# Kernel tuning notes

Hardware: AMD Instinct MI355X
Metric: run time of the kernel (lower is better)

## Reference

```python
import jax, jax.numpy as jnp
import numpy as np

N = 100000      # n_nodes
D = 64          # in_features (= out_features)
H = 4           # attention heads
DK = D // H     # per-head dim
E = 1600000     # num edges (avg degree 16)
STEP = 0.25     # ODE euler step size
NSTEPS = 4      # integrate t in [0, 1]
ALPHA = 0.2     # LeakyReLU negative slope


def setup_inputs() -> dict:
    key = jax.random.key(0)
    k1, k2, k3, k4 = jax.random.split(key, 4)
    x = jax.random.normal(k1, (N, D), dtype=jnp.float32)
    edge_index = jax.random.randint(k2, (2, E), 0, N, dtype=jnp.int32)
    edge_weight = jax.random.uniform(k3, (E,), dtype=jnp.float32)
    # HamAgg.weight: init.eye_ -> identity [D, D]
    W = jnp.eye(D, dtype=jnp.float32)
    # HAM_GATConv.a: xavier_normal_ on shape (2*d_k, 1, 1), gain=1.414
    a = jax.random.normal(k4, (2 * DK,), dtype=jnp.float32) * (1.414 * np.sqrt(2.0 / (2 * DK + 1)))
    return {"x": x, "edge_index": edge_index, "edge_weight": edge_weight, "W": W, "a": a}


def reference(x, edge_index, edge_weight, W, a):
    # ---- Hamiltonian ODE block (args.vt == 'fc', odemap 'h1extend') ----
    # xt = hstack([x, x @ W.T]); euler-integrate canonical Hamiltonian flow
    # dq/dt = p, dp/dt = -q over t in [0,1] with step 0.25; keep first D dims.
    q = x
    p = x @ W.T
    for _ in range(NSTEPS):
        q, p = q + STEP * p, p - STEP * q
    xt = q  # out_x = out[..., :D]

    row, col = edge_index[0], edge_index[1]

    # ---- HAM_GATConv attention (W_x = x @ I = x) ----
    # h[n, head, k] = xt[n, head*DK + k]
    h = xt.reshape(N, H, DK)
    a_src, a_dst = a[:DK], a[DK:]
    s_src = h @ a_src   # [N, H] per-node source contribution
    s_dst = h @ a_dst   # [N, H] per-node dest contribution
    score = jax.nn.leaky_relu(s_src[row] + s_dst[col], ALPHA)  # [E, H]

    # segment softmax grouped by destination (edge[1])
    seg_max = jax.ops.segment_max(score, col, num_segments=N)  # [N, H]
    seg_max = jnp.where(jnp.isfinite(seg_max), seg_max, 0.0)
    e = jnp.exp(score - seg_max[col])
    denom = jax.ops.segment_sum(e, col, num_segments=N)
    att = e / (denom[col] + 1e-16)  # [E, H]

    # ---- mean over heads of per-head spmm == single spmm with mean attention ----
    # spmm: out[row[e]] += att[e] * xt[col[e]]
    w = att.mean(axis=1)  # [E]
    out = jax.ops.segment_sum(w[:, None] * xt[col], row, num_segments=N)  # [N, D]
    return out
```

## Files before the change

### kernel.cpp

```cpp
#include <hip/hip_runtime.h>
#include <hip/hip_bf16.h>


#define LRELU(v) ((v) > 0.0f ? (v) : 0.2f * (v))

#define EC 4096
#define BSC 256
#define BSR 128
#define DS 4
#define SLOTS 4

typedef __attribute__((ext_vector_type(8))) short bf16x8;
typedef __attribute__((ext_vector_type(4))) float f32x4;

__device__ __forceinline__ float bf16_to_f32(unsigned short u) {
    return __uint_as_float((unsigned int)u << 16);
}
__device__ __forceinline__ float bflo(unsigned int u) {
    return __uint_as_float(u << 16);
}
__device__ __forceinline__ float bfhi(unsigned int u) {
    return __uint_as_float(u & 0xFFFF0000u);
}
__device__ __forceinline__ unsigned short f32_to_bf16(float f) {
    __hip_bfloat16 h = __float2bfloat16(f);
    return *reinterpret_cast<unsigned short*>(&h);
}

__global__ __launch_bounds__(256) void k_front(const float* __restrict__ x,
                                               const float* __restrict__ W,
                                               const float* __restrict__ a,
                                               const int* __restrict__ row,
                                               const int* __restrict__ col,
                                               unsigned short* __restrict__ xt16,
                                               float* __restrict__ s_src,
                                               float* __restrict__ s_dst,
                                               int* __restrict__ Hr,
                                               int* __restrict__ Hc,
                                               int n, int e, int nbn, int nblk,
                                               int nbr, int nbc,
                                               float c1, float c2) {
    __shared__ unsigned short geffL[16 * 64];
    __shared__ int hr[1024];
    __shared__ int hc[512];
    int t = threadIdx.x;
    if (blockIdx.x < nbn) {
        {
            int k = t & 63, h = t >> 6;
            float ssrc = 0.0f, sdst = 0.0f;
#pragma unroll
            for (int d = 0; d < 16; ++d) {
                float w = W[(h * 16 + d) * 64 + k];
                ssrc += w * a[d];
                sdst += w * a[16 + d];
            }
            float gsrc = c2 * ssrc, gdst = c2 * sdst;
            if ((k >> 4) == h) {
                gsrc += c1 * a[k & 15];
                gdst += c1 * a[16 + (k & 15)];
            }
            unsigned short sh = f32_to_bf16(gsrc);
            unsigned short sl = f32_to_bf16(gsrc - bf16_to_f32(sh));
            unsigned short dh = f32_to_bf16(gdst);
            unsigned short dl = f32_to_bf16(gdst - bf16_to_f32(dh));
            geffL[h * 64 + k] = sh;
            geffL[(4 + h) * 64 + k] = dh;
            geffL[(8 + h) * 64 + k] = sl;
            geffL[(12 + h) * 64 + k] = dl;
        }
        __syncthreads();

        int wave = t >> 6;
        int lane = t & 63;
        int nb = blockIdx.x * 64 + wave * 16;
        if (nb >= n) return;
        int colg = lane & 15;
        int grp = lane >> 4;
        int k0 = grp << 3;

        bf16x8 wf[4][2];
#pragma unroll
        for (int ct = 0; ct < 4; ++ct) {
#pragma unroll
            for (int ks = 0; ks < 2; ++ks) {
                const float* wr = W + (size_t)(ct * 16 + colg) * 64 + k0 + ks * 32;
                float4 w0 = *(const float4*)(wr);
                float4 w1 = *(const float4*)(wr + 4);
                bf16x8 f;
                f[0] = (short)f32_to_bf16(w0.x); f[1] = (short)f32_to_bf16(w0.y);
                f[2] = (short)f32_to_bf16(w0.z); f[3] = (short)f32_to_bf16(w0.w);
                f[4] = (short)f32_to_bf16(w1.x); f[5] = (short)f32_to_bf16(w1.y);
                f[6] = (short)f32_to_bf16(w1.z); f[7] = (short)f32_to_bf16(w1.w);
                wf[ct][ks] = f;
            }
        }
        bf16x8 gf[2];
#pragma unroll
        for (int ks = 0; ks < 2; ++ks)
            gf[ks] = *(const bf16x8*)(geffL + colg * 64 + k0 + ks * 32);

        int arow = nb + colg;
        if (arow >= n) arow = n - 1;
        const float* xr = x + (size_t)arow * 64 + k0;
        bf16x8 af[2];
#pragma unroll
        for (int ks = 0; ks < 2; ++ks) {
            float4 x0 = *(const float4*)(xr + ks * 32);
            float4 x1 = *(const float4*)(xr + ks * 32 + 4);
            bf16x8 f;
            f[0] = (short)f32_to_bf16(x0.x); f[1] = (short)f32_to_bf16(x0.y);
            f[2] = (short)f32_to_bf16(x0.z); f[3] = (short)f32_to_bf16(x0.w);
            f[4] = (short)f32_to_bf16(x1.x); f[5] = (short)f32_to_bf16(x1.y);
            f[6] = (short)f32_to_bf16(x1.z); f[7] = (short)f32_to_bf16(x1.w);
            af[ks] = f;
        }

        f32x4 acc[5];
#pragma unroll
        for (int i = 0; i < 5; ++i) acc[i] = (f32x4){0.f, 0.f, 0.f, 0.f};
#pragma unroll
        for (int ct = 0; ct < 4; ++ct) {
            acc[ct] = __builtin_amdgcn_mfma_f32_16x16x32_bf16(af[0], wf[ct][0], acc[ct], 0, 0, 0);
            acc[ct] = __builtin_amdgcn_mfma_f32_16x16x32_bf16(af[1], wf[ct][1], acc[ct], 0, 0, 0);
        }
        acc[4] = __builtin_amdgcn_mfma_f32_16x16x32_bf16(af[0], gf[0], acc[4], 0, 0, 0);
        acc[4] = __builtin_amdgcn_mfma_f32_16x16x32_bf16(af[1], gf[1], acc[4], 0, 0, 0);

#pragma unroll
        for (int ct = 0; ct < 4; ++ct) {
            int c = ct * 16 + colg;
#pragma unroll
            for (int rr = 0; rr < 4; ++rr) {
                int node = nb + grp * 4 + rr;
                if (node < n) {
                    float xv = x[(size_t)node * 64 + c];
                    float xtv = c1 * xv + c2 * acc[ct][rr];
                    xt16[(size_t)node * 64 + c] = f32_to_bf16(xtv);
                }
            }
        }
#pragma unroll
        for (int rr = 0; rr < 4; ++rr) {
            float v = acc[4][rr];
            float tot = v + __shfl_xor(v, 8, 64);
            int node = nb + grp * 4 + rr;
            if (node < n) {
                if (colg < 4) s_src[node * 4 + colg] = tot;
                else if (colg < 8) s_dst[node * 4 + (colg - 4)] = tot;
            }
        }
    } else {
        int blk = blockIdx.x - nbn;
        for (int i = t; i < 1024; i += 256) hr[i] = 0;
        for (int i = t; i < 512; i += 256) hc[i] = 0;
        __syncthreads();
        int base = blk * EC;
#pragma unroll
        for (int j = 0; j < EC / 256; ++j) {
            int i = base + t + j * 256;
            if (i < e) {
                atomicAdd(&hr[row[i] >> 7], 1);
                atomicAdd(&hc[col[i] >> 8], 1);
            }
        }
        __syncthreads();
        for (int b = t; b < nbr; b += 256) Hr[(size_t)b * nblk + blk] = hr[b];
        for (int b = t; b < nbc; b += 256) Hc[(size_t)b * nblk + blk] = hc[b];
    }
}

__global__ __launch_bounds__(256) void k_scanH2(int* __restrict__ Hr,
                                                int* __restrict__ Hc,
                                                int* __restrict__ BtotR,
                                                int* __restrict__ BtotC,
                                                int nblk, int nbr) {
    __shared__ int vals[512];
    __shared__ int part[256];
    int t = threadIdx.x;
    int bb = blockIdx.x;
    int* Hb;
    int* Btot;
    if (bb < nbr) {
        Hb = Hr + (size_t)bb * nblk;
        Btot = BtotR + bb;
    } else {
        Hb = Hc + (size_t)(bb - nbr) * nblk;
        Btot = BtotC + (bb - nbr);
    }
    for (int i = t; i < nblk; i += 256) vals[i] = Hb[i];
    __syncthreads();
    int c0 = t * 2;
    int s = 0;
#pragma unroll
    for (int j = 0; j < 2; ++j)
        if (c0 + j < nblk) s += vals[c0 + j];
    part[t] = s;
    __syncthreads();
    for (int d = 1; d < 256; d <<= 1) {
        int add = (t >= d) ? part[t - d] : 0;
        __syncthreads();
        part[t] += add;
        __syncthreads();
    }
    int run = part[t] - s;
#pragma unroll
    for (int j = 0; j < 2; ++j) {
        int i = c0 + j;
        if (i < nblk) {
            int v = vals[i];
            Hb[i] = run;
            run += v;
        }
    }
    if (t == 255) *Btot = part[255];
}

__global__ __launch_bounds__(256) void k_scatter_dual(
    const int* __restrict__ row, const int* __restrict__ col,
    const int* __restrict__ Hr, const int* __restrict__ Hc,
    const int* __restrict__ BtotR, const int* __restrict__ BtotC,
    int* __restrict__ BbR, int* __restrict__ BbC,
    int* __restrict__ ebr, int* __restrict__ ebc,
    int e, int nblk, int nbr, int nbc) {
    __shared__ int vals[1024];
    __shared__ int part[256];
    __shared__ int curr[1024];
    __shared__ int curc[512];
    int t = threadIdx.x;
    int blk = blockIdx.x;
    for (int i = t; i < nbr; i += 256) vals[i] = BtotR[i];
    __syncthreads();
    {
        int c0 = t * 4, s = 0;
#pragma unroll
        for (int j = 0; j < 4; ++j)
            if (c0 + j < nbr) s += vals[c0 + j];
        part[t] = s;
        __syncthreads();
        for (int d = 1; d < 256; d <<= 1) {
            int add = (t >= d) ? part[t - d] : 0;
            __syncthreads();
            part[t] += add;
            __syncthreads();
        }
        int run = part[t] - s;
#pragma unroll
        for (int j = 0; j < 4; ++j) {
            int i = c0 + j;
            if (i < nbr) {
                int v = vals[i];
                curr[i] = run + Hr[(size_t)i * nblk + blk];
                if (blk == 0) BbR[i] = run;
                run += v;
            }
        }
        if (blk == 0 && t == 255) BbR[nbr] = part[255];
    }
    __syncthreads();
    for (int i = t; i < nbc; i += 256) vals[i] = BtotC[i];
    __syncthreads();
    {
        int c0 = t * 4, s = 0;
#pragma unroll
        for (int j = 0; j < 4; ++j)
            if (c0 + j < nbc) s += vals[c0 + j];
        part[t] = s;
        __syncthreads();
        for (int d = 1; d < 256; d <<= 1) {
            int add = (t >= d) ? part[t - d] : 0;
            __syncthreads();
            part[t] += add;
            __syncthreads();
        }
        int run = part[t] - s;
#pragma unroll
        for (int j = 0; j < 4; ++j) {
            int i = c0 + j;
            if (i < nbc) {
                int v = vals[i];
                curc[i] = run + Hc[(size_t)i * nblk + blk];
                if (blk == 0) BbC[i] = run;
                run += v;
            }
        }
        if (blk == 0 && t == 255) BbC[nbc] = part[255];
    }
    __syncthreads();
    int base = blk * EC;
#pragma unroll
    for (int j = 0; j < EC / 256; ++j) {
        int i = base + t + j * 256;
        if (i < e) {
            int r = row[i], c = col[i];
            int pr = atomicAdd(&curr[r >> 7], 1);
            ebr[pr] = (c << 7) | (r & 127);
            int pc = atomicAdd(&curc[c >> 8], 1);
            ebc[pc] = (r << 8) | (c & 255);
        }
    }
}

__global__ __launch_bounds__(256) void k_denom_p(const int* __restrict__ ebc,
                                                 const int* __restrict__ BbC,
                                                 const float* __restrict__ s_src,
                                                 const float* __restrict__ s_dst,
                                                 float* __restrict__ part,
                                                 int n, int n4) {
    __shared__ float acc[BSC * 4];
    __shared__ float sd[BSC * 4];
    int t = threadIdx.x;
    int bucket = blockIdx.x >> 2;
    int slice = blockIdx.x & 3;
    int cbase = bucket << 8;
    for (int i = t; i < BSC * 4; i += 256) {
        acc[i] = 0.0f;
        int c4 = cbase * 4 + i;
        sd[i] = (c4 < n4) ? s_dst[c4] : 0.0f;
    }
    __syncthreads();
    int start = BbC[bucket], end = BbC[bucket + 1];
    int len = end - start;
    int i0 = start + (int)(((long long)len * slice) >> 2);
    int i1 = start + (int)(((long long)len * (slice + 1)) >> 2);
    for (int i = i0 + t; i < i1; i += 256) {
        int p = ebc[i];
        int r = p >> 8, cl = p & 255;
        float4 ss = *(const float4*)(s_src + (size_t)r * 4);
        atomicAdd(&acc[cl * 4 + 0], __expf(LRELU(ss.x + sd[cl * 4 + 0])));
        atomicAdd(&acc[cl * 4 + 1], __expf(LRELU(ss.y + sd[cl * 4 + 1])));
        atomicAdd(&acc[cl * 4 + 2], __expf(LRELU(ss.z + sd[cl * 4 + 2])));
        atomicAdd(&acc[cl * 4 + 3], __expf(LRELU(ss.w + sd[cl * 4 + 3])));
    }
    __syncthreads();
    float* ps = part + (size_t)slice * n4;
    for (int i = t; i < BSC * 4; i += 256) {
        int c4 = cbase * 4 + i;
        if (c4 < n4) ps[c4] = acc[i];
    }
}

__global__ __launch_bounds__(256) void k_comb(const float* __restrict__ part,
                                              const float* __restrict__ s_dst,
                                              float* __restrict__ sdr, int n4) {
    int idx = blockIdx.x * 256 + threadIdx.x;
    if (idx >= n4) return;
    float s = part[idx] + part[(size_t)n4 + idx] + part[(size_t)2 * n4 + idx] +
              part[(size_t)3 * n4 + idx];
    int c = idx >> 2, h = idx & 3;
    sdr[(size_t)c * 8 + h] = s_dst[idx];
    sdr[(size_t)c * 8 + 4 + h] = 1.0f / (s + 1e-16f);
}

__global__ __launch_bounds__(256) void k_sort2(const int* __restrict__ ebr,
                                               const int* __restrict__ BbR,
                                               const float* __restrict__ s_src,
                                               const float* __restrict__ sdr,
                                               int* __restrict__ rowptr,
                                               int2* __restrict__ cwp,
                                               int n, int e) {
    __shared__ int cnt[BSR];
    __shared__ int pfx[BSR];
    __shared__ int cur[BSR];
    __shared__ float ssh[BSR * 4];
    int t = threadIdx.x;
    int b = blockIdx.x;
    int rbase = b << 7;
    if (t < BSR) cnt[t] = 0;
    for (int i = t; i < BSR * 4; i += 256) {
        int g = rbase * 4 + i;
        ssh[i] = (g < n * 4) ? s_src[g] : 0.0f;
    }
    __syncthreads();
    int start = BbR[b], end = BbR[b + 1];
    for (int i = start + t; i < end; i += 256)
        atomicAdd(&cnt[ebr[i] & 127], 1);
    __syncthreads();
    if (t < BSR) pfx[t] = cnt[t];
    __syncthreads();
    for (int d = 1; d < BSR; d <<= 1) {
        int v = (t < BSR && t >= d) ? pfx[t - d] : 0;
        __syncthreads();
        if (t < BSR) pfx[t] += v;
        __syncthreads();
    }
    if (t < BSR) {
        int excl = start + pfx[t] - cnt[t];
        cur[t] = excl;
        int r = rbase + t;
        if (r < n) rowptr[r] = excl;
    }
    if (b == 0 && t == 0) rowptr[n] = e;
    __syncthreads();
    for (int i = start + t; i < end; i += 256) {
        int p = ebr[i];
        int rl = p & 127, c = p >> 7;
        float4 sd = *(const float4*)(sdr + (size_t)c * 8);
        float4 rd = *(const float4*)(sdr + (size_t)c * 8 + 4);
        float wv = __expf(LRELU(ssh[rl * 4 + 0] + sd.x)) * rd.x +
                   __expf(LRELU(ssh[rl * 4 + 1] + sd.y)) * rd.y +
                   __expf(LRELU(ssh[rl * 4 + 2] + sd.z)) * rd.z +
                   __expf(LRELU(ssh[rl * 4 + 3] + sd.w)) * rd.w;
        int pos = atomicAdd(&cur[rl], 1);
        cwp[pos] = make_int2(c << 6, __float_as_int(0.25f * wv));
    }
}

__global__ __launch_bounds__(256) void k_aggr(const int* __restrict__ rowptr,
                                              const int2* __restrict__ cwp,
                                              const unsigned short* __restrict__ xt16,
                                              float* __restrict__ out, int n, int e) {
    int r = blockIdx.x * 4 + (threadIdx.x >> 6);
    if (r >= n) return;
    int lane = threadIdx.x & 63;
    int g = lane >> 3;
    unsigned le = (lane & 7) << 3;
    int start = rowptr[r], end = rowptr[r + 1];
    float acc[8];
#pragma unroll
    for (int j = 0; j < 8; ++j) acc[j] = 0.0f;
    for (int base = start; base < end; base += SLOTS * 8) {
        int m = end - base;
        if (m > SLOTS * 8) m = SLOTS * 8;
        int nk = (m + 7) >> 3;
        uint4 u[SLOTS];
        float wv[SLOTS];
#pragma unroll
        for (int k = 0; k < SLOTS; ++k) {
            if (k < nk) {
                int idx = base + k * 8 + g;
                int idc = idx < e ? idx : e - 1;
                int2 cw = cwp[idc];
                wv[k] = (idx < end) ? __int_as_float(cw.y) : 0.0f;
                u[k] = *(const uint4*)(xt16 + ((unsigned)cw.x + le));
            }
        }
#pragma unroll
        for (int k = 0; k < SLOTS; ++k) {
            if (k < nk) {
                acc[0] = fmaf(wv[k], bflo(u[k].x), acc[0]);
                acc[1] = fmaf(wv[k], bfhi(u[k].x), acc[1]);
                acc[2] = fmaf(wv[k], bflo(u[k].y), acc[2]);
                acc[3] = fmaf(wv[k], bfhi(u[k].y), acc[3]);
                acc[4] = fmaf(wv[k], bflo(u[k].z), acc[4]);
                acc[5] = fmaf(wv[k], bfhi(u[k].z), acc[5]);
                acc[6] = fmaf(wv[k], bflo(u[k].w), acc[6]);
                acc[7] = fmaf(wv[k], bfhi(u[k].w), acc[7]);
            }
        }
    }
#pragma unroll
    for (int off = 8; off <= 32; off <<= 1) {
#pragma unroll
        for (int j = 0; j < 8; ++j) acc[j] += __shfl_xor(acc[j], off, 64);
    }
    if (lane < 8) {
        float4 a0 = {acc[0], acc[1], acc[2], acc[3]};
        float4 a1 = {acc[4], acc[5], acc[6], acc[7]};
        *(float4*)(out + (size_t)r * 64 + le) = a0;
        *(float4*)(out + (size_t)r * 64 + le + 4) = a1;
    }
}

extern "C" void kernel_launch(void* const* d_in, const int* in_sizes, int n_in,
                              void* d_out, int out_size, void* d_ws, size_t ws_size,
                              hipStream_t stream) {
    const float* x = (const float*)d_in[0];
    const int* ei = (const int*)d_in[1];
    const float* W = (const float*)d_in[3];
    const float* a = (const float*)d_in[4];
    int n = in_sizes[0] / 64;
    int e = in_sizes[1] / 2;
    const int* row = ei;
    const int* col = ei + e;
    float* out = (float*)d_out;

    int nblk = (e + EC - 1) / EC;
    int nbr = (n + BSR - 1) / BSR;
    int nbc = (n + BSC - 1) / BSC;
    int nbn = (n + 63) / 64;
    int n4 = n * 4;

    size_t o = 0;
    auto take = [&](size_t cnt) {
        size_t p = o;
        o += (cnt + 3) & ~(size_t)3;
        return p;
    };
    int* wsi = (int*)d_ws;
    unsigned short* xt16 = (unsigned short*)(wsi + take((size_t)n * 32));
    float* s_src = (float*)(wsi + take((size_t)n * 4));
    float* s_dst = (float*)(wsi + take((size_t)n * 4));
    float* sdr = (float*)(wsi + take((size_t)n * 8));
    float* part = (float*)(wsi + take((size_t)n * 4 * DS));
    int* Hr = wsi + take((size_t)nbr * nblk);
    int* Hc = wsi + take((size_t)nbc * nblk);
    int* BtotR = wsi + take(nbr);
    int* BbR = wsi + take(nbr + 1);
    int* BtotC = wsi + take(nbc);
    int* BbC = wsi + take(nbc + 1);
    int* ebr = wsi + take(e);
    int* cwbuf = wsi + take((size_t)2 * e);
    int* ebc = cwbuf;
    int2* cwp = (int2*)cwbuf;
    int* rowptr = wsi + take(n + 1);

    float aq = 1.f, bq = 0.f, ap = 0.f, bp = 1.f;
    for (int i = 0; i < 4; ++i) {
        float naq = aq + 0.25f * ap, nbq = bq + 0.25f * bp;
        float nap = ap - 0.25f * aq, nbp = bp - 0.25f * bq;
        aq = naq; bq = nbq; ap = nap; bp = nbp;
    }

    k_front<<<nbn + nblk, 256, 0, stream>>>(x, W, a, row, col, xt16, s_src,
                                            s_dst, Hr, Hc, n, e, nbn, nblk,
                                            nbr, nbc, aq, bq);
    k_scanH2<<<nbr + nbc, 256, 0, stream>>>(Hr, Hc, BtotR, BtotC, nblk, nbr);
    k_scatter_dual<<<nblk, 256, 0, stream>>>(row, col, Hr, Hc, BtotR, BtotC,
                                             BbR, BbC, ebr, ebc, e, nblk,
                                             nbr, nbc);
    k_denom_p<<<nbc * DS, 256, 0, stream>>>(ebc, BbC, s_src, s_dst, part, n, n4);
    k_comb<<<(n4 + 255) / 256, 256, 0, stream>>>(part, s_dst, sdr, n4);
    k_sort2<<<nbr, 256, 0, stream>>>(ebr, BbR, s_src, sdr, rowptr, cwp, n, e);
    k_aggr<<<(n + 3) / 4, 256, 0, stream>>>(rowptr, cwp, xt16, out, n, e);
}
```

Baseline: 281.3 us.

## Halve histogram chunk size and move row counting into the denominator kernel

The edge histogram in the front kernel now uses 2048-edge chunks, giving twice as many histogram blocks for more parallelism. The scatter kernel still works on 4096-edge chunks and reads every other histogram column, and the scan kernel handles up to 1024 entries per bucket. The per-row counting and prefix-sum that used to open the sort kernel now runs as extra blocks inside the denominator kernel, so it executes concurrently with the softmax denominator work. The placement kernel then only reads the precomputed rowptr. The cost is more histogram writes, plus a second pass over ebr in a separate kernel.

```diff
diff --git a/kernel.cpp b/kernel.cpp
--- a/kernel.cpp
+++ b/kernel.cpp
@@ -5,6 +5,7 @@
 #define LRELU(v) ((v) > 0.0f ? (v) : 0.2f * (v))
 
 #define EC 4096
+#define ECH 2048
 #define BSC 256
 #define BSR 128
 #define DS 4
@@ -37,7 +38,7 @@
                                                float* __restrict__ s_dst,
                                                int* __restrict__ Hr,
                                                int* __restrict__ Hc,
-                                               int n, int e, int nbn, int nblk,
+                                               int n, int e, int nbn, int nblkH,
                                                int nbr, int nbc,
                                                float c1, float c2) {
     __shared__ unsigned short geffL[16 * 64];
@@ -154,9 +155,9 @@
         for (int i = t; i < 1024; i += 256) hr[i] = 0;
         for (int i = t; i < 512; i += 256) hc[i] = 0;
         __syncthreads();
-        int base = blk * EC;
-#pragma unroll
-        for (int j = 0; j < EC / 256; ++j) {
+        int base = blk * ECH;
+#pragma unroll
+        for (int j = 0; j < ECH / 256; ++j) {
             int i = base + t + j * 256;
             if (i < e) {
                 atomicAdd(&hr[row[i] >> 7], 1);
@@ -164,8 +165,8 @@
             }
         }
         __syncthreads();
-        for (int b = t; b < nbr; b += 256) Hr[(size_t)b * nblk + blk] = hr[b];
-        for (int b = t; b < nbc; b += 256) Hc[(size_t)b * nblk + blk] = hc[b];
+        for (int b = t; b < nbr; b += 256) Hr[(size_t)b * nblkH + blk] = hr[b];
+        for (int b = t; b < nbc; b += 256) Hc[(size_t)b * nblkH + blk] = hc[b];
     }
 }
 
@@ -173,27 +174,27 @@
                                                 int* __restrict__ Hc,
                                                 int* __restrict__ BtotR,
                                                 int* __restrict__ BtotC,
-                                                int nblk, int nbr) {
-    __shared__ int vals[512];
+                                                int nblkH, int nbr) {
+    __shared__ int vals[1024];
     __shared__ int part[256];
     int t = threadIdx.x;
     int bb = blockIdx.x;
     int* Hb;
     int* Btot;
     if (bb < nbr) {
-        Hb = Hr + (size_t)bb * nblk;
+        Hb = Hr + (size_t)bb * nblkH;
         Btot = BtotR + bb;
     } else {
-        Hb = Hc + (size_t)(bb - nbr) * nblk;
+        Hb = Hc + (size_t)(bb - nbr) * nblkH;
         Btot = BtotC + (bb - nbr);
     }
-    for (int i = t; i < nblk; i += 256) vals[i] = Hb[i];
-    __syncthreads();
-    int c0 = t * 2;
+    for (int i = t; i < nblkH; i += 256) vals[i] = Hb[i];
+    __syncthreads();
+    int c0 = t * 4;
     int s = 0;
 #pragma unroll
-    for (int j = 0; j < 2; ++j)
-        if (c0 + j < nblk) s += vals[c0 + j];
+    for (int j = 0; j < 4; ++j)
+        if (c0 + j < nblkH) s += vals[c0 + j];
     part[t] = s;
     __syncthreads();
     for (int d = 1; d < 256; d <<= 1) {
@@ -204,9 +205,9 @@
     }
     int run = part[t] - s;
 #pragma unroll
-    for (int j = 0; j < 2; ++j) {
+    for (int j = 0; j < 4; ++j) {
         int i = c0 + j;
-        if (i < nblk) {
+        if (i < nblkH) {
             int v = vals[i];
             Hb[i] = run;
             run += v;
@@ -221,13 +222,14 @@
     const int* __restrict__ BtotR, const int* __restrict__ BtotC,
     int* __restrict__ BbR, int* __restrict__ BbC,
     int* __restrict__ ebr, int* __restrict__ ebc,
-    int e, int nblk, int nbr, int nbc) {
+    int e, int nblkH, int nbr, int nbc) {
     __shared__ int vals[1024];
     __shared__ int part[256];
     __shared__ int curr[1024];
     __shared__ int curc[512];
     int t = threadIdx.x;
     int blk = blockIdx.x;
+    int hcol = blk << 1;
     for (int i = t; i < nbr; i += 256) vals[i] = BtotR[i];
     __syncthreads();
     {
@@ -249,7 +251,7 @@
             int i = c0 + j;
             if (i < nbr) {
                 int v = vals[i];
-                curr[i] = run + Hr[(size_t)i * nblk + blk];
+                curr[i] = run + Hr[(size_t)i * nblkH + hcol];
                 if (blk == 0) BbR[i] = run;
                 run += v;
             }
@@ -278,7 +280,7 @@
             int i = c0 + j;
             if (i < nbc) {
                 int v = vals[i];
-                curc[i] = run + Hc[(size_t)i * nblk + blk];
+                curc[i] = run + Hc[(size_t)i * nblkH + hcol];
                 if (blk == 0) BbC[i] = run;
                 run += v;
             }
@@ -300,42 +302,71 @@
     }
 }
 
-__global__ __launch_bounds__(256) void k_denom_p(const int* __restrict__ ebc,
-                                                 const int* __restrict__ BbC,
-                                                 const float* __restrict__ s_src,
-                                                 const float* __restrict__ s_dst,
-                                                 float* __restrict__ part,
-                                                 int n, int n4) {
+__global__ __launch_bounds__(256) void k_mid(const int* __restrict__ ebc,
+                                             const int* __restrict__ BbC,
+                                             const int* __restrict__ ebr,
+                                             const int* __restrict__ BbR,
+                                             const float* __restrict__ s_src,
+                                             const float* __restrict__ s_dst,
+                                             float* __restrict__ part,
+                                             int* __restrict__ rowptr,
+                                             int n, int n4, int e, int ndenom) {
     __shared__ float acc[BSC * 4];
     __shared__ float sd[BSC * 4];
+    __shared__ int cnt[BSR];
+    __shared__ int pfx[BSR];
     int t = threadIdx.x;
-    int bucket = blockIdx.x >> 2;
-    int slice = blockIdx.x & 3;
-    int cbase = bucket << 8;
-    for (int i = t; i < BSC * 4; i += 256) {
-        acc[i] = 0.0f;
-        int c4 = cbase * 4 + i;
-        sd[i] = (c4 < n4) ? s_dst[c4] : 0.0f;
-    }
-    __syncthreads();
-    int start = BbC[bucket], end = BbC[bucket + 1];
-    int len = end - start;
-    int i0 = start + (int)(((long long)len * slice) >> 2);
-    int i1 = start + (int)(((long long)len * (slice + 1)) >> 2);
-    for (int i = i0 + t; i < i1; i += 256) {
-        int p = ebc[i];
-        int r = p >> 8, cl = p & 255;
-        float4 ss = *(const float4*)(s_src + (size_t)r * 4);
-        atomicAdd(&acc[cl * 4 + 0], __expf(LRELU(ss.x + sd[cl * 4 + 0])));
-        atomicAdd(&acc[cl * 4 + 1], __expf(LRELU(ss.y + sd[cl * 4 + 1])));
-        atomicAdd(&acc[cl * 4 + 2], __expf(LRELU(ss.z + sd[cl * 4 + 2])));
-        atomicAdd(&acc[cl * 4 + 3], __expf(LRELU(ss.w + sd[cl * 4 + 3])));
-    }
-    __syncthreads();
-    float* ps = part + (size_t)slice * n4;
-    for (int i = t; i < BSC * 4; i += 256) {
-        int c4 = cbase * 4 + i;
-        if (c4 < n4) ps[c4] = acc[i];
+    if (blockIdx.x < ndenom) {
+        int bucket = blockIdx.x >> 2;
+        int slice = blockIdx.x & 3;
+        int cbase = bucket << 8;
+        for (int i = t; i < BSC * 4; i += 256) {
+            acc[i] = 0.0f;
+            int c4 = cbase * 4 + i;
+            sd[i] = (c4 < n4) ? s_dst[c4] : 0.0f;
+        }
+        __syncthreads();
+        int start = BbC[bucket], end = BbC[bucket + 1];
+        int len = end - start;
+        int i0 = start + (int)(((long long)len * slice) >> 2);
+        int i1 = start + (int)(((long long)len * (slice + 1)) >> 2);
+        for (int i = i0 + t; i < i1; i += 256) {
+            int p = ebc[i];
+            int r = p >> 8, cl = p & 255;
+            float4 ss = *(const float4*)(s_src + (size_t)r * 4);
+            atomicAdd(&acc[cl * 4 + 0], __expf(LRELU(ss.x + sd[cl * 4 + 0])));
+            atomicAdd(&acc[cl * 4 + 1], __expf(LRELU(ss.y + sd[cl * 4 + 1])));
+            atomicAdd(&acc[cl * 4 + 2], __expf(LRELU(ss.z + sd[cl * 4 + 2])));
+            atomicAdd(&acc[cl * 4 + 3], __expf(LRELU(ss.w + sd[cl * 4 + 3])));
+        }
+        __syncthreads();
+        float* ps = part + (size_t)slice * n4;
+        for (int i = t; i < BSC * 4; i += 256) {
+            int c4 = cbase * 4 + i;
+            if (c4 < n4) ps[c4] = acc[i];
+        }
+    } else {
+        int b = blockIdx.x - ndenom;
+        int rbase = b << 7;
+        if (t < BSR) cnt[t] = 0;
+        __syncthreads();
+        int start = BbR[b], end = BbR[b + 1];
+        for (int i = start + t; i < end; i += 256)
+            atomicAdd(&cnt[ebr[i] & 127], 1);
+        __syncthreads();
+        if (t < BSR) pfx[t] = cnt[t];
+        __syncthreads();
+        for (int d = 1; d < BSR; d <<= 1) {
+            int v = (t < BSR && t >= d) ? pfx[t - d] : 0;
+            __syncthreads();
+            if (t < BSR) pfx[t] += v;
+            __syncthreads();
+        }
+        if (t < BSR) {
+            int r = rbase + t;
+            if (r < n) rowptr[r] = start + pfx[t] - cnt[t];
+        }
+        if (b == 0 && t == 0) rowptr[n] = e;
     }
 }
 
@@ -351,46 +382,25 @@
     sdr[(size_t)c * 8 + 4 + h] = 1.0f / (s + 1e-16f);
 }
 
-__global__ __launch_bounds__(256) void k_sort2(const int* __restrict__ ebr,
+__global__ __launch_bounds__(256) void k_place(const int* __restrict__ ebr,
                                                const int* __restrict__ BbR,
                                                const float* __restrict__ s_src,
                                                const float* __restrict__ sdr,
-                                               int* __restrict__ rowptr,
+                                               const int* __restrict__ rowptr,
                                                int2* __restrict__ cwp,
                                                int n, int e) {
-    __shared__ int cnt[BSR];
-    __shared__ int pfx[BSR];
     __shared__ int cur[BSR];
     __shared__ float ssh[BSR * 4];
     int t = threadIdx.x;
     int b = blockIdx.x;
     int rbase = b << 7;
-    if (t < BSR) cnt[t] = 0;
+    if (t < BSR) cur[t] = rowptr[min(rbase + t, n)];
     for (int i = t; i < BSR * 4; i += 256) {
         int g = rbase * 4 + i;
         ssh[i] = (g < n * 4) ? s_src[g] : 0.0f;
     }
     __syncthreads();
     int start = BbR[b], end = BbR[b + 1];
-    for (int i = start + t; i < end; i += 256)
-        atomicAdd(&cnt[ebr[i] & 127], 1);
-    __syncthreads();
-    if (t < BSR) pfx[t] = cnt[t];
-    __syncthreads();
-    for (int d = 1; d < BSR; d <<= 1) {
-        int v = (t < BSR && t >= d) ? pfx[t - d] : 0;
-        __syncthreads();
-        if (t < BSR) pfx[t] += v;
-        __syncthreads();
-    }
-    if (t < BSR) {
-        int excl = start + pfx[t] - cnt[t];
-        cur[t] = excl;
-        int r = rbase + t;
-        if (r < n) rowptr[r] = excl;
-    }
-    if (b == 0 && t == 0) rowptr[n] = e;
-    __syncthreads();
     for (int i = start + t; i < end; i += 256) {
         int p = ebr[i];
         int rl = p & 127, c = p >> 7;
@@ -475,10 +485,12 @@
     float* out = (float*)d_out;
 
     int nblk = (e + EC - 1) / EC;
+    int nblkH = (e + ECH - 1) / ECH;
     int nbr = (n + BSR - 1) / BSR;
     int nbc = (n + BSC - 1) / BSC;
     int nbn = (n + 63) / 64;
     int n4 = n * 4;
+    int ndenom = nbc * DS;
 
     size_t o = 0;
     auto take = [&](size_t cnt) {
@@ -492,8 +504,8 @@
     float* s_dst = (float*)(wsi + take((size_t)n * 4));
     float* sdr = (float*)(wsi + take((size_t)n * 8));
     float* part = (float*)(wsi + take((size_t)n * 4 * DS));
-    int* Hr = wsi + take((size_t)nbr * nblk);
-    int* Hc = wsi + take((size_t)nbc * nblk);
+    int* Hr = wsi + take((size_t)nbr * nblkH);
+    int* Hc = wsi + take((size_t)nbc * nblkH);
     int* BtotR = wsi + take(nbr);
     int* BbR = wsi + take(nbr + 1);
     int* BtotC = wsi + take(nbc);
@@ -511,15 +523,16 @@
         aq = naq; bq = nbq; ap = nap; bp = nbp;
     }
 
-    k_front<<<nbn + nblk, 256, 0, stream>>>(x, W, a, row, col, xt16, s_src,
-                                            s_dst, Hr, Hc, n, e, nbn, nblk,
-                                            nbr, nbc, aq, bq);
-    k_scanH2<<<nbr + nbc, 256, 0, stream>>>(Hr, Hc, BtotR, BtotC, nblk, nbr);
+    k_front<<<nbn + nblkH, 256, 0, stream>>>(x, W, a, row, col, xt16, s_src,
+                                             s_dst, Hr, Hc, n, e, nbn, nblkH,
+                                             nbr, nbc, aq, bq);
+    k_scanH2<<<nbr + nbc, 256, 0, stream>>>(Hr, Hc, BtotR, BtotC, nblkH, nbr);
     k_scatter_dual<<<nblk, 256, 0, stream>>>(row, col, Hr, Hc, BtotR, BtotC,
-                                             BbR, BbC, ebr, ebc, e, nblk,
+                                             BbR, BbC, ebr, ebc, e, nblkH,
                                              nbr, nbc);
-    k_denom_p<<<nbc * DS, 256, 0, stream>>>(ebc, BbC, s_src, s_dst, part, n, n4);
+    k_mid<<<ndenom + nbr, 256, 0, stream>>>(ebc, BbC, ebr, BbR, s_src, s_dst,
+                                            part, rowptr, n, n4, e, ndenom);
     k_comb<<<(n4 + 255) / 256, 256, 0, stream>>>(part, s_dst, sdr, n4);
-    k_sort2<<<nbr, 256, 0, stream>>>(ebr, BbR, s_src, sdr, rowptr, cwp, n, e);
+    k_place<<<nbr, 256, 0, stream>>>(ebr, BbR, s_src, sdr, rowptr, cwp, n, e);
     k_aggr<<<(n + 3) / 4, 256, 0, stream>>>(rowptr, cwp, xt16, out, n, e);
 }
```

After: 288.5 us. +2.6%, slower.
